# Kernel optimization log

Hardware: AMD Instinct MI355X
Metric: run time of the kernel (lower is better)

The kernel has to match this reference:

```python
import jax, jax.numpy as jnp
import numpy as np

LAT_MIN, LAT_MAX = -90.0, 90.0
LON_MIN, LON_MAX = 0.0, 360.0
N_LEVELS = 4
N_FEAT = 2
FINEST = 0.25
BASE = 1.0
LAT_SHAPE, LON_SHAPE = 720, 1440
GEODESIC_WEIGHT = True
TABLE = (LAT_SHAPE + 1) * (LON_SHAPE + 1)  # 1038961
# corner offsets in the torch BOX_OFFSETS order: (0,0),(0,1),(1,0),(1,1)
OFFS = np.array([[0, 0], [0, 1], [1, 0], [1, 1]], dtype=np.int32)


def setup_inputs() -> dict:
    key = jax.random.key(0)
    k1, k2 = jax.random.split(key)
    B = 2_000_000
    u = jax.random.uniform(k1, (B, 2), dtype=jnp.float32)
    # lat in [-90, 90), lon in [0, 360)
    x = jnp.stack([u[:, 0] * 180.0 - 90.0, u[:, 1] * 360.0], axis=1)
    embeddings = jax.random.uniform(k2, (N_LEVELS, TABLE, N_FEAT),
                                    minval=-1e-4, maxval=1e-4, dtype=jnp.float32)
    return {"x": x, "embeddings": embeddings}


def _geodesic(lat1, lon1, lat2, lon2):
    r = jnp.pi / 180.0
    rl1, rl2 = lat1 * r, lat2 * r
    dlat = (lat2 - lat1) * r
    dlon = (lon2 - lon1) * r
    a = jnp.sin(dlat / 2) ** 2 + jnp.cos(rl1) * jnp.cos(rl2) * jnp.sin(dlon / 2) ** 2
    return 2.0 * jnp.arctan2(jnp.sqrt(a), jnp.sqrt(1.0 - a))


def reference(x, embeddings):
    box_min = jnp.array([LAT_MIN - FINEST, LON_MIN - FINEST], dtype=x.dtype)
    box_max = jnp.array([LAT_MAX + FINEST, LON_MAX + FINEST], dtype=x.dtype)
    xc = jnp.clip(x, box_min, box_max)  # clamped coords used for grid indexing
    offs = jnp.asarray(OFFS)
    outs = []
    for i in range(N_LEVELS):
        gs = BASE * (2.0 ** i)  # grid size (same for lat and lon)
        bl = jnp.floor((xc - box_min) / gs).astype(jnp.int32)  # [B,2] bottom-left idx
        gmin = bl.astype(x.dtype) * gs + box_min                # [B,2]
        gmax = gmin + gs
        width = int(np.floor(LON_SHAPE / gs))
        # 4 corner flat indices: lat_idx * width + lon_idx -> [B,4]
        idx = (bl[:, 0:1] + offs[None, :, 0]) * width + (bl[:, 1:2] + offs[None, :, 1])
        e = embeddings[i][idx]  # gather: [B,4,F]
        if GEODESIC_WEIGHT:
            wlat = _geodesic(gmin[:, 0], gmin[:, 1], x[:, 0], gmin[:, 1]) / \
                   _geodesic(gmin[:, 0], gmin[:, 1], gmax[:, 0], gmin[:, 1])
            wlon = _geodesic(gmin[:, 0], x[:, 1], gmin[:, 0], gmax[:, 1]) / \
                   _geodesic(gmin[:, 0], gmin[:, 1], gmin[:, 0], gmax[:, 1])
        else:
            w = (x - gmin) / (gmax - gmin)
            wlat, wlon = w[:, 0], w[:, 1]
        # bilinear blend (corner order: 0=(0,0) 1=(0,1) 2=(1,0) 3=(1,1))
        c0 = e[:, 0] * (1 - wlat[:, None]) + e[:, 2] * wlat[:, None]
        c1 = e[:, 1] * (1 - wlat[:, None]) + e[:, 3] * wlat[:, None]
        outs.append(c0 * (1 - wlon[:, None]) + c1 * wlon[:, None])
    return jnp.concatenate(outs, axis=-1)  # [B, N_LEVELS*N_FEAT]
```

## Files before the change

kernel.cpp:

```cpp
#include <hip/hip_runtime.h>

#define NT 1024

constexpr int TABLE_SZ = 721 * 1441;

constexpr int W2 = 92, H2 = 47;
constexpr int W3 = 47, H3 = 24;

typedef float v4f __attribute__((ext_vector_type(4)));

__global__ __launch_bounds__(NT)
void ngp_interp_kernel(const float* __restrict__ x,
                       const float* __restrict__ emb,
                       float* __restrict__ out,
                       int B)
{
    __shared__ float2 lds2[H2 * W2];
    __shared__ float2 lds3[H3 * W3];

    const float2* embv = reinterpret_cast<const float2*>(emb);
    for (int t = threadIdx.x; t < H2 * W2; t += NT) {
        int lat = t / W2, lon = t - lat * W2;
        lds2[t] = embv[(size_t)2 * TABLE_SZ + lat * 360 + lon];
    }
    for (int t = threadIdx.x; t < H3 * W3; t += NT) {
        int lat = t / W3, lon = t - lat * W3;
        lds3[t] = embv[(size_t)3 * TABLE_SZ + lat * 180 + lon];
    }
    __syncthreads();

    const int p = blockIdx.x * NT + threadIdx.x;
    if (p >= B) return;

    const float xlat = __builtin_nontemporal_load(x + (size_t)p * 2);
    const float xlon = __builtin_nontemporal_load(x + (size_t)p * 2 + 1);

    const float bmin_lat = -90.25f, bmax_lat = 90.25f;
    const float bmin_lon = -0.25f,  bmax_lon = 360.25f;
    const float xc_lat = fminf(fmaxf(xlat, bmin_lat), bmax_lat);
    const float xc_lon = fminf(fmaxf(xlon, bmin_lon), bmax_lon);

    const float r = 0.017453292519943295f;
    const float s2_tab[4] = {0.008726535498f, 0.017452406437f,
                             0.034899496703f, 0.069756473744f};

    float o[8];

    #pragma unroll
    for (int i = 0; i < 4; ++i) {
        const float gs     = (float)(1 << i);
        const float inv_gs = 1.0f / gs;
        const int   width  = 1440 >> i;

        const float blat_f = floorf((xc_lat - bmin_lat) * inv_gs);
        const float blon_f = floorf((xc_lon - bmin_lon) * inv_gs);
        const float gmin_lat = blat_f * gs + bmin_lat;
        const float gmin_lon = blon_f * gs + bmin_lon;
        const float gmax_lon = gmin_lon + gs;
        const int bl_lat = (int)blat_f;
        const int bl_lon = (int)blon_f;

        float2 e0, e1, e2, e3;
        if (i == 0 || i == 1) {
            const int idx00 = bl_lat * width + bl_lon;
            const float* base0 = emb + ((size_t)i * TABLE_SZ + (size_t)idx00) * 2;
            const float* base1 = base0 + (size_t)width * 2;
            v4f eA, eB;
            __builtin_memcpy(&eA, base0, 16);
            __builtin_memcpy(&eB, base1, 16);
            e0 = make_float2(eA.x, eA.y); e1 = make_float2(eA.z, eA.w);
            e2 = make_float2(eB.x, eB.y); e3 = make_float2(eB.z, eB.w);
        } else if (i == 2) {
            const int c = bl_lat * W2 + bl_lon;
            e0 = lds2[c];      e1 = lds2[c + 1];
            e2 = lds2[c + W2]; e3 = lds2[c + W2 + 1];
        } else {
            const int c = bl_lat * W3 + bl_lon;
            e0 = lds3[c];      e1 = lds3[c + 1];
            e2 = lds3[c + W3]; e3 = lds3[c + W3 + 1];
        }

        const float wlat = (xlat - gmin_lat) * inv_gs;

        const float ca = fabsf(__cosf(gmin_lat * r));
        const float h1 = (gmax_lon - xlon) * r * 0.5f;
        const float s1 = h1 - h1 * h1 * h1 * (1.0f / 6.0f);
        const float z1 = ca * s1;
        const float z2 = ca * s2_tab[i];
        const float n1 = z1 + z1 * z1 * z1 * (1.0f / 6.0f);
        const float n2 = z2 + z2 * z2 * z2 * (1.0f / 6.0f);
        const float wlon = n1 * __builtin_amdgcn_rcpf(n2);

        const float c0x = e0.x + (e2.x - e0.x) * wlat;
        const float c0y = e0.y + (e2.y - e0.y) * wlat;
        const float c1x = e1.x + (e3.x - e1.x) * wlat;
        const float c1y = e1.y + (e3.y - e1.y) * wlat;
        o[2*i]   = c0x + (c1x - c0x) * wlon;
        o[2*i+1] = c0y + (c1y - c0y) * wlon;
    }

    v4f* op = reinterpret_cast<v4f*>(out + (size_t)p * 8);
    v4f lo = {o[0], o[1], o[2], o[3]};
    v4f hi = {o[4], o[5], o[6], o[7]};
    __builtin_nontemporal_store(lo, op);
    __builtin_nontemporal_store(hi, op + 1);
}

extern "C" void kernel_launch(void* const* d_in, const int* in_sizes, int n_in,
                              void* d_out, int out_size, void* d_ws, size_t ws_size,
                              hipStream_t stream)
{
    const float* x   = (const float*)d_in[0];
    const float* emb = (const float*)d_in[1];
    float* out = (float*)d_out;
    const int B = in_sizes[0] / 2;
    const int grid = (B + NT - 1) / NT;
    ngp_interp_kernel<<<grid, NT, 0, stream>>>(x, emb, out, B);
}
```

Before: 134.5 us.

## Prebuild packed level-0/1 corner quads per coarse cell in workspace

Adds a pre-pass kernel that, for each 1-degree cell, packs the four level-0 corners and the four level-1 corners into one contiguous 64-byte record in the workspace. The main kernel then fetches levels 0 and 1 with four consecutive 16-byte loads from a single record instead of four scattered loads across two tables. The input point is also read as one 8-byte vector load. This trades an extra kernel launch that writes about 4 MB for fewer scattered gather transactions and less address arithmetic per point. The packed path is only taken when the workspace is large enough.

```diff
diff --git a/kernel.cpp b/kernel.cpp
--- a/kernel.cpp
+++ b/kernel.cpp
@@ -7,11 +7,41 @@
 constexpr int W2 = 92, H2 = 47;
 constexpr int W3 = 47, H3 = 24;
 
+constexpr int QLAT = 181, QLON = 361;
+constexpr int NCELLS = QLAT * QLON;
+
 typedef float v4f __attribute__((ext_vector_type(4)));
+typedef float v2f __attribute__((ext_vector_type(2)));
 
+__global__ __launch_bounds__(256)
+void build_superquad(const float* __restrict__ emb, float* __restrict__ sq)
+{
+    int c = blockIdx.x * 256 + threadIdx.x;
+    if (c >= NCELLS) return;
+    int la = c / QLON, lo = c - la * QLON;
+    const float2* t0 = (const float2*)emb;
+    const float2* t1 = t0 + TABLE_SZ;
+    float2 a0 = t0[la * 1440 + lo];
+    float2 a1 = t0[la * 1440 + lo + 1];
+    float2 a2 = t0[(la + 1) * 1440 + lo];
+    float2 a3 = t0[(la + 1) * 1440 + lo + 1];
+    int la1 = la >> 1, lo1 = lo >> 1;
+    float2 b0 = t1[la1 * 720 + lo1];
+    float2 b1 = t1[la1 * 720 + lo1 + 1];
+    float2 b2 = t1[(la1 + 1) * 720 + lo1];
+    float2 b3 = t1[(la1 + 1) * 720 + lo1 + 1];
+    v4f* o = (v4f*)(sq + (size_t)c * 16);
+    o[0] = (v4f){a0.x, a0.y, a1.x, a1.y};
+    o[1] = (v4f){a2.x, a2.y, a3.x, a3.y};
+    o[2] = (v4f){b0.x, b0.y, b1.x, b1.y};
+    o[3] = (v4f){b2.x, b2.y, b3.x, b3.y};
+}
+
+template <bool USE_SQ>
 __global__ __launch_bounds__(NT)
 void ngp_interp_kernel(const float* __restrict__ x,
                        const float* __restrict__ emb,
+                       const float* __restrict__ sq,
                        float* __restrict__ out,
                        int B)
 {
@@ -32,8 +62,9 @@
     const int p = blockIdx.x * NT + threadIdx.x;
     if (p >= B) return;
 
-    const float xlat = __builtin_nontemporal_load(x + (size_t)p * 2);
-    const float xlon = __builtin_nontemporal_load(x + (size_t)p * 2 + 1);
+    const v2f xp = __builtin_nontemporal_load(reinterpret_cast<const v2f*>(x) + p);
+    const float xlat = xp.x;
+    const float xlon = xp.y;
 
     const float bmin_lat = -90.25f, bmax_lat = 90.25f;
     const float bmin_lon = -0.25f,  bmax_lon = 360.25f;
@@ -44,6 +75,11 @@
     const float s2_tab[4] = {0.008726535498f, 0.017452406437f,
                              0.034899496703f, 0.069756473744f};
 
+    const float v_lat = xc_lat - bmin_lat;
+    const float v_lon = xc_lon - bmin_lon;
+    const int cell0 = (int)floorf(v_lat) * QLON + (int)floorf(v_lon);
+    const v4f* sqv = reinterpret_cast<const v4f*>(sq) + (size_t)cell0 * 4;
+
     float o[8];
 
     #pragma unroll
@@ -52,32 +88,38 @@
         const float inv_gs = 1.0f / gs;
         const int   width  = 1440 >> i;
 
-        const float blat_f = floorf((xc_lat - bmin_lat) * inv_gs);
-        const float blon_f = floorf((xc_lon - bmin_lon) * inv_gs);
+        const float blat_f = floorf(v_lat * inv_gs);
+        const float blon_f = floorf(v_lon * inv_gs);
         const float gmin_lat = blat_f * gs + bmin_lat;
         const float gmin_lon = blon_f * gs + bmin_lon;
         const float gmax_lon = gmin_lon + gs;
         const int bl_lat = (int)blat_f;
         const int bl_lon = (int)blon_f;
 
-        float2 e0, e1, e2, e3;
-        if (i == 0 || i == 1) {
-            const int idx00 = bl_lat * width + bl_lon;
-            const float* base0 = emb + ((size_t)i * TABLE_SZ + (size_t)idx00) * 2;
-            const float* base1 = base0 + (size_t)width * 2;
-            v4f eA, eB;
-            __builtin_memcpy(&eA, base0, 16);
-            __builtin_memcpy(&eB, base1, 16);
-            e0 = make_float2(eA.x, eA.y); e1 = make_float2(eA.z, eA.w);
-            e2 = make_float2(eB.x, eB.y); e3 = make_float2(eB.z, eB.w);
+        v4f eA, eB;
+        if (i <= 1) {
+            if (USE_SQ) {
+                eA = sqv[2 * i];
+                eB = sqv[2 * i + 1];
+            } else {
+                const int idx00 = bl_lat * width + bl_lon;
+                const float* base0 = emb + ((size_t)i * TABLE_SZ + (size_t)idx00) * 2;
+                const float* base1 = base0 + (size_t)width * 2;
+                __builtin_memcpy(&eA, base0, 16);
+                __builtin_memcpy(&eB, base1, 16);
+            }
         } else if (i == 2) {
             const int c = bl_lat * W2 + bl_lon;
-            e0 = lds2[c];      e1 = lds2[c + 1];
-            e2 = lds2[c + W2]; e3 = lds2[c + W2 + 1];
+            float2 e0 = lds2[c],      e1 = lds2[c + 1];
+            float2 e2 = lds2[c + W2], e3 = lds2[c + W2 + 1];
+            eA = (v4f){e0.x, e0.y, e1.x, e1.y};
+            eB = (v4f){e2.x, e2.y, e3.x, e3.y};
         } else {
             const int c = bl_lat * W3 + bl_lon;
-            e0 = lds3[c];      e1 = lds3[c + 1];
-            e2 = lds3[c + W3]; e3 = lds3[c + W3 + 1];
+            float2 e0 = lds3[c],      e1 = lds3[c + 1];
+            float2 e2 = lds3[c + W3], e3 = lds3[c + W3 + 1];
+            eA = (v4f){e0.x, e0.y, e1.x, e1.y};
+            eB = (v4f){e2.x, e2.y, e3.x, e3.y};
         }
 
         const float wlat = (xlat - gmin_lat) * inv_gs;
@@ -91,10 +133,10 @@
         const float n2 = z2 + z2 * z2 * z2 * (1.0f / 6.0f);
         const float wlon = n1 * __builtin_amdgcn_rcpf(n2);
 
-        const float c0x = e0.x + (e2.x - e0.x) * wlat;
-        const float c0y = e0.y + (e2.y - e0.y) * wlat;
-        const float c1x = e1.x + (e3.x - e1.x) * wlat;
-        const float c1y = e1.y + (e3.y - e1.y) * wlat;
+        const float c0x = eA.x + (eB.x - eA.x) * wlat;
+        const float c0y = eA.y + (eB.y - eA.y) * wlat;
+        const float c1x = eA.z + (eB.z - eA.z) * wlat;
+        const float c1y = eA.w + (eB.w - eA.w) * wlat;
         o[2*i]   = c0x + (c1x - c0x) * wlon;
         o[2*i+1] = c0y + (c1y - c0y) * wlon;
     }
@@ -115,5 +157,13 @@
     float* out = (float*)d_out;
     const int B = in_sizes[0] / 2;
     const int grid = (B + NT - 1) / NT;
-    ngp_interp_kernel<<<grid, NT, 0, stream>>>(x, emb, out, B);
+
+    const size_t sq_bytes = (size_t)NCELLS * 64;
+    if (ws_size >= sq_bytes) {
+        float* sq = (float*)d_ws;
+        build_superquad<<<(NCELLS + 255) / 256, 256, 0, stream>>>(emb, sq);
+        ngp_interp_kernel<true><<<grid, NT, 0, stream>>>(x, emb, sq, out, B);
+    } else {
+        ngp_interp_kernel<false><<<grid, NT, 0, stream>>>(x, emb, nullptr, out, B);
+    }
 }
```

Result: faster. 128.3 us (-4.7%).
